# Kernel tuning notes

Measured on AMD Instinct MI355X. Metric: run time of the kernel, lower is better.

Reference implementation:

```python
import jax, jax.numpy as jnp
import numpy as np

N = 2048      # n_nodes
D = 512       # n_channels
AVG_DEG = 16  # average graph degree


def setup_inputs() -> dict:
    key = jax.random.key(0)
    k1, k2, k3 = jax.random.split(key, 3)
    # node features [N, D]
    x = jax.random.normal(k1, (N, D), dtype=jnp.float32)
    # random symmetric graph -> combinatorial Laplacian L = D - A
    E = N * AVG_DEG
    src = jax.random.randint(k2, (E,), 0, N)
    dst = jax.random.randint(k3, (E,), 0, N)
    A = jnp.zeros((N, N), jnp.float32).at[src, dst].add(1.0)
    A = (A + A.T) * 0.5
    A = A * (1.0 - jnp.eye(N, dtype=jnp.float32))  # drop self loops
    deg = A.sum(axis=1)
    L = jnp.diag(deg) - A
    # learned diffusion time (scalar parameter, ic=0.5)
    t = jnp.float32(0.5)
    return {"x": x, "L": L, "t": t}


def reference(x, L, t):
    # forward clamps diffusion_time to >= 1e-8
    tt = jnp.maximum(t, jnp.float32(1e-8))
    # heat kernel: expm(-t * L); the original loops over channels applying
    # compute_diffusion(x[:, [i]], t, L, 'matrix_exp') == expm(-t L) @ x[:, i],
    # which is exactly one dense matmul fused across all channels.
    P = jax.scipy.linalg.expm(-tt * L)  # [N, N]
    return P @ x  # [N, D]
```

## Files before the change

### kernel.cpp

```cpp
#include <hip/hip_runtime.h>

#define N_NODES 2048
#define N_CH    512
#define K_CHEB  48
#define NB      256

#define OFF_DIAG   0
#define OFF_BASE   20480
#define OFF_CNTO   28672
#define OFF_BND    36868
#define OFF_PKV    40960

#define PAD_OFF    16384u

__device__ __forceinline__ float b2f(unsigned short u) {
    return __uint_as_float(((unsigned int)u) << 16);
}
__device__ __forceinline__ bool detect32(const unsigned int* tw) {
    return (tw[0] & 0xFFFFu) == 0u;
}

__global__ void __launch_bounds__(256)
k_prep(const void* __restrict__ Lp, const unsigned int* __restrict__ tw,
       float* __restrict__ diagv, int* __restrict__ basev, int* __restrict__ cnto,
       unsigned short* __restrict__ pkv, unsigned int* __restrict__ bnd) {
    __shared__ unsigned short stage[4][N_NODES];
    __shared__ int scnt[4];
    int w    = threadIdx.x >> 6;
    int lane = threadIdx.x & 63;
    int row  = blockIdx.x * 4 + w;
    if (blockIdx.x == 0 && threadIdx.x == 0) *bnd = 0u;
    bool is32 = detect32(tw);
    int run = 0; float dv = 0.f;
    if (is32) {
        const float4* rf4 = (const float4*)((const float*)Lp + (size_t)row * N_NODES);
        #pragma unroll
        for (int i = 0; i < 8; i++) {
            int j = i * 64 + lane;
            float4 v = rf4[j];
            if (j == (row >> 2)) {
                int rm = row & 3;
                if      (rm == 0) { dv = v.x; v.x = 0.f; }
                else if (rm == 1) { dv = v.y; v.y = 0.f; }
                else if (rm == 2) { dv = v.z; v.z = 0.f; }
                else              { dv = v.w; v.w = 0.f; }
            }
            int c0 = j * 4;
            int n0 = (v.x != 0.f) ? (int)(-2.0f * v.x + 0.5f) : 0;
            int n1 = (v.y != 0.f) ? (int)(-2.0f * v.y + 0.5f) : 0;
            int n2 = (v.z != 0.f) ? (int)(-2.0f * v.z + 0.5f) : 0;
            int n3 = (v.w != 0.f) ? (int)(-2.0f * v.w + 0.5f) : 0;
            int tn = n0 + n1 + n2 + n3;
            int xs = tn;
            #pragma unroll
            for (int d = 1; d < 64; d <<= 1) { int q = __shfl_up(xs, d); if (lane >= d) xs += q; }
            int o = run + xs - tn;
            for (int q = 0; q < n0; q++) stage[w][o++] = (unsigned short)((c0 + 0) << 3);
            for (int q = 0; q < n1; q++) stage[w][o++] = (unsigned short)((c0 + 1) << 3);
            for (int q = 0; q < n2; q++) stage[w][o++] = (unsigned short)((c0 + 2) << 3);
            for (int q = 0; q < n3; q++) stage[w][o++] = (unsigned short)((c0 + 3) << 3);
            run += __shfl(xs, 63);
        }
    } else {
        const unsigned short* rp = (const unsigned short*)Lp + (size_t)row * N_NODES;
        for (int c0 = 0; c0 < N_NODES; c0 += 64) {
            float v = b2f(rp[c0 + lane]);
            int n = 0;
            if (c0 + lane == row) dv = v;
            else if (v != 0.f)    n = (int)(-2.0f * v + 0.5f);
            int xs = n;
            #pragma unroll
            for (int d = 1; d < 64; d <<= 1) { int q = __shfl_up(xs, d); if (lane >= d) xs += q; }
            int o = run + xs - n;
            for (int q = 0; q < n; q++) stage[w][o + q] = (unsigned short)((c0 + lane) << 3);
            run += __shfl(xs, 63);
        }
    }
    #pragma unroll
    for (int o = 32; o; o >>= 1) dv += __shfl_xor(dv, o);
    int padded = (run + 7) & ~7;
    for (int e = run + lane; e < padded; e += 64) stage[w][e] = (unsigned short)PAD_OFF;
    if (lane == 0) scnt[w] = padded;
    __syncthreads();
    int myb = blockIdx.x * 256;
    for (int w2 = 0; w2 < w; w2++) myb += scnt[w2];
    if (lane == 0) { basev[row] = myb; cnto[row] = padded >> 3; diagv[row] = dv; }
    const unsigned int* s32 = (const unsigned int*)stage[w];
    unsigned int* p32 = (unsigned int*)pkv + (myb >> 1);
    for (int i = lane; i < (padded >> 1); i += 64) p32[i] = s32[i];
}

__global__ void __launch_bounds__(256)
k_bound(const float* __restrict__ diagv, const int* __restrict__ basev,
        const int* __restrict__ cnto, const unsigned short* __restrict__ pkv,
        unsigned int* __restrict__ bnd) {
    __shared__ float wmax[4];
    int w    = threadIdx.x >> 6;
    int lane = threadIdx.x & 63;
    int r    = blockIdx.x * 4 + w;
    float d = diagv[r];
    float mb = 0.f;
    if (d > 0.f) {
        const unsigned short* pe = pkv + basev[r];
        int cnt = cnto[r] << 3;
        float s = 0.f;
        for (int e = lane; e < cnt; e += 64) {
            unsigned int u = pe[e];
            if (u < PAD_OFF) s += diagv[u >> 3];
        }
        #pragma unroll
        for (int o = 32; o; o >>= 1) s += __shfl_xor(s, o);
        mb = d + 0.5f * s / d;
    }
    if (lane == 0) wmax[w] = mb;
    __syncthreads();
    if (threadIdx.x == 0) {
        float m = fmaxf(fmaxf(wmax[0], wmax[1]), fmaxf(wmax[2], wmax[3]));
        atomicMax(bnd, __float_as_uint(m));
    }
}

__device__ __forceinline__ void oct_acc(const float2* __restrict__ cur, uint4 q,
                                        float& ax, float& ay, float& bx, float& by) {
    const char* cb = (const char*)cur;
    #pragma unroll
    for (int i = 0; i < 4; i++) {
        unsigned int u = (i == 0) ? q.x : (i == 1) ? q.y : (i == 2) ? q.z : q.w;
        float2 c0 = *(const float2*)(cb + (u & 0xFFFFu));
        float2 c1 = *(const float2*)(cb + (u >> 16));
        ax += c0.x; ay += c0.y;
        bx += c1.x; by += c1.y;
    }
}

__device__ __forceinline__ float2 gatherR(const float2* __restrict__ cur,
                                          const uint4* __restrict__ s4,
                                          int j0, int j1) {
    float ax = 0.f, ay = 0.f, bx = 0.f, by = 0.f;
    int j = j0;
    if (j + 2 <= j1) {
        uint4 q0 = s4[j], q1 = s4[j + 1];
        j += 2;
        while (j + 2 <= j1) {
            uint4 p0 = s4[j], p1 = s4[j + 1];
            oct_acc(cur, q0, ax, ay, bx, by);
            oct_acc(cur, q1, ax, ay, bx, by);
            q0 = p0; q1 = p1;
            j += 2;
        }
        oct_acc(cur, q0, ax, ay, bx, by);
        oct_acc(cur, q1, ax, ay, bx, by);
    }
    if (j < j1) oct_acc(cur, s4[j], ax, ay, bx, by);
    return make_float2(ax + bx, ay + by);
}

__global__ void __launch_bounds__(1024, 4)
k_cheb(const void* __restrict__ x, const unsigned int* __restrict__ tw,
       const int* __restrict__ basev, const int* __restrict__ cnto,
       const float* __restrict__ diagv, const unsigned short* __restrict__ pkv,
       const unsigned int* __restrict__ bnd, void* __restrict__ out) {
    __shared__ float2 bufA[N_NODES + 8];
    __shared__ float2 bufB[N_NODES + 8];
    __shared__ float  scoef[K_CHEB + 1];
    __shared__ float  cabs[K_CHEB + 1];
    __shared__ int    permL[N_NODES];
    __shared__ int    waveCnt[16][32];
    __shared__ int    wavePre[16][32];
    __shared__ int    hstart[32];
    __shared__ float  sred[16];
    __shared__ double dzs;
    __shared__ float  gss;
    __shared__ int    kks;

    int t    = threadIdx.x;
    int lane = t & 63;
    int wid  = t >> 6;
    int cb   = blockIdx.x * 2;
    bool is32 = detect32(tw);
    if (t == 0) {
        bufA[N_NODES] = make_float2(0.f, 0.f);
        bufB[N_NODES] = make_float2(0.f, 0.f);
    }
    int r0 = t, r1 = t + 1024;
    float mx = fmaxf(diagv[r0], diagv[r1]);
    int q0 = min(cnto[r0], 31), q1 = min(cnto[r1], 31);
    unsigned long long below = (1ull << lane) - 1ull;
    int rk0 = 0, rk1 = 0;
    #pragma unroll 1
    for (int k = 0; k < 32; k++) {
        unsigned long long m0 = __ballot(q0 == k);
        unsigned long long m1 = __ballot(q1 == k);
        if (q0 == k) rk0 = (int)__popcll(m0 & below);
        if (q1 == k) rk1 = (int)__popcll(m0) + (int)__popcll(m1 & below);
        if (lane == 0) waveCnt[wid][k] = (int)(__popcll(m0) + __popcll(m1));
    }
    #pragma unroll
    for (int o = 32; o; o >>= 1) mx = fmaxf(mx, __shfl_xor(mx, o));
    if (lane == 0) sred[wid] = mx;
    __syncthreads();
    if (t < 32) {
        int acc = 0;
        for (int w2 = 0; w2 < 16; w2++) { wavePre[w2][t] = acc; acc += waveCnt[w2][t]; }
        hstart[t] = acc;
    }
    __syncthreads();
    if (t == 0) {
        int acc = 0;
        for (int l = 31; l >= 0; l--) { int c = hstart[l]; hstart[l] = acc; acc += c; }
        float m = sred[0];
        #pragma unroll
        for (int i = 1; i < 16; i++) m = fmaxf(m, sred[i]);
        float tt = is32 ? __uint_as_float(tw[0]) : b2f((unsigned short)(tw[0] & 0xFFFFu));
        tt = fmaxf(tt, 1e-8f);
        float beta = 2.0f * m;
        float bM   = __uint_as_float(bnd[0]) * 1.00002f + 1e-7f;
        if (bM > 0.f && bM < beta) beta = bM;
        gss = (beta > 0.f) ? 2.0f / beta : 0.f;
        dzs = (beta > 0.f) ? (double)tt * (double)beta * 0.5 : 0.0;
    }
    __syncthreads();
    if (t <= K_CHEB) {
        int k = t;
        double z = dzs;
        double emz = exp(-z), h = 0.5 * z, h2 = h * h;
        double term = 1.0;
        for (int j = 1; j <= k; j++) term *= h / (double)j;
        double sum = term;
        for (int m = 1; m < 300; m++) {
            term *= h2 / ((double)m * (double)(m + k));
            sum += term;
            if (term == 0.0 || term < sum * 1e-18) break;
        }
        double ck = emz * sum * (k == 0 ? 1.0 : 2.0);
        if (k & 1) ck = -ck;
        scoef[k] = (float)ck;
        cabs[k]  = (float)fabs(ck);
    }
    permL[hstart[q0] + wavePre[wid][q0] + rk0] = r0;
    permL[hstart[q1] + wavePre[wid][q1] + rk1] = r1;
    __syncthreads();
    if (t == 0) {
        int keff = 1;
        for (int k = K_CHEB; k >= 2; k--)
            if (cabs[k] >= 2.5e-4f) { keff = k; break; }
        kks = keff;
    }
    __syncthreads();

    int ra = permL[t], rb = permL[2047 - t];
    int na = cnto[ra], nb = cnto[rb];
    int ja = basev[ra] >> 3, jb = basev[rb] >> 3;
    const uint4* s4 = (const uint4*)pkv;
    float da = diagv[ra], db = diagv[rb];
    float g = gss;
    int   K = kks;

    float2 xa, xb;
    if (is32) {
        xa = *(const float2*)((const float*)x + (size_t)ra * N_CH + cb);
        xb = *(const float2*)((const float*)x + (size_t)rb * N_CH + cb);
    } else {
        const unsigned short* xp = (const unsigned short*)x;
        unsigned int wa = *(const unsigned int*)(xp + (size_t)ra * N_CH + cb);
        unsigned int wb = *(const unsigned int*)(xp + (size_t)rb * N_CH + cb);
        xa = make_float2(b2f((unsigned short)(wa & 0xFFFFu)), b2f((unsigned short)(wa >> 16)));
        xb = make_float2(b2f((unsigned short)(wb & 0xFFFFu)), b2f((unsigned short)(wb >> 16)));
    }
    bufA[ra] = xa; bufA[rb] = xb;
    __syncthreads();

    float gm = -0.5f * g;
    float ia = g * da - 1.f, ib = g * db - 1.f;
    float2 aa = gatherR(bufA, s4, ja, ja + na);
    float2 ab = gatherR(bufA, s4, jb, jb + nb);
    float2 pva = xa, pvb = xb;
    float2 cua = make_float2(gm * aa.x + ia * xa.x, gm * aa.y + ia * xa.y);
    float2 cub = make_float2(gm * ab.x + ib * xb.x, gm * ab.y + ib * xb.y);
    float c0 = scoef[0], c1 = scoef[1];
    float2 oa = make_float2(c0 * xa.x + c1 * cua.x, c0 * xa.y + c1 * cua.y);
    float2 ob = make_float2(c0 * xb.x + c1 * cub.x, c0 * xb.y + c1 * cub.y);
    bufB[ra] = cua; bufB[rb] = cub;
    __syncthreads();

    float gn  = -g;
    float dga = 2.f * g * da - 2.f, dgb = 2.f * g * db - 2.f;

#define CHEB_STEP(RD, WR)                                                  \
    {   float ck = scoef[k];                                               \
        float2 ba = gatherR(RD, s4, ja, ja + na);                          \
        float2 bb = gatherR(RD, s4, jb, jb + nb);                          \
        float2 tna = make_float2(gn * ba.x + dga * cua.x - pva.x,          \
                                 gn * ba.y + dga * cua.y - pva.y);         \
        float2 tnb = make_float2(gn * bb.x + dgb * cub.x - pvb.x,          \
                                 gn * bb.y + dgb * cub.y - pvb.y);         \
        pva = cua; cua = tna;                                              \
        pvb = cub; cub = tnb;                                              \
        oa.x += ck * tna.x; oa.y += ck * tna.y;                            \
        ob.x += ck * tnb.x; ob.y += ck * tnb.y;                            \
        WR[ra] = tna; WR[rb] = tnb;                                        \
        __syncthreads(); }

    int k = 2;
    while (k <= K) {
        CHEB_STEP(bufB, bufA)
        k++;
        if (k > K) break;
        CHEB_STEP(bufA, bufB)
        k++;
    }
#undef CHEB_STEP

    if (is32) {
        *(float2*)((float*)out + (size_t)ra * N_CH + cb) = oa;
        *(float2*)((float*)out + (size_t)rb * N_CH + cb) = ob;
    } else {
        unsigned int ua, ub;
        { unsigned int u0 = __float_as_uint(oa.x), u1 = __float_as_uint(oa.y);
          u0 = (u0 + 0x7FFFu + ((u0 >> 16) & 1u)) >> 16;
          u1 = (u1 + 0x7FFFu + ((u1 >> 16) & 1u)) >> 16;
          ua = u0 | (u1 << 16); }
        { unsigned int u0 = __float_as_uint(ob.x), u1 = __float_as_uint(ob.y);
          u0 = (u0 + 0x7FFFu + ((u0 >> 16) & 1u)) >> 16;
          u1 = (u1 + 0x7FFFu + ((u1 >> 16) & 1u)) >> 16;
          ub = u0 | (u1 << 16); }
        *(unsigned int*)((unsigned short*)out + (size_t)ra * N_CH + cb) = ua;
        *(unsigned int*)((unsigned short*)out + (size_t)rb * N_CH + cb) = ub;
    }
}

extern "C" void kernel_launch(void* const* d_in, const int* in_sizes, int n_in,
                              void* d_out, int out_size, void* d_ws, size_t ws_size,
                              hipStream_t stream) {
    const void* x  = d_in[0];
    const void* L  = d_in[1];
    const void* tp = d_in[2];
    const unsigned int* tw = (const unsigned int*)tp;

    char* ws = (char*)d_ws;
    float*          diagv = (float*)          (ws + OFF_DIAG);
    int*            basev = (int*)            (ws + OFF_BASE);
    int*            cnto  = (int*)            (ws + OFF_CNTO);
    unsigned int*   bnd   = (unsigned int*)   (ws + OFF_BND);
    unsigned short* pkv   = (unsigned short*) (ws + OFF_PKV);

    k_prep <<<512, 256, 0, stream>>>(L, tw, diagv, basev, cnto, pkv, bnd);
    k_bound<<<512, 256, 0, stream>>>(diagv, basev, cnto, pkv, bnd);
    k_cheb <<<NB, 1024, 0, stream>>>(x, tw, basev, cnto, diagv, pkv, bnd, d_out);
}
```

Before: 164.0 us.

## Fold spectral bound computation into Chebyshev kernel and remap channel blocks

Removes the separate k_bound launch and recomputes the Gershgorin-style spectral bound redundantly inside every k_cheb block, reduced with wave shuffles and shared memory instead of a global atomicMax. A zero sentinel is written at diagv[N_NODES] so pad entries index a zero diagonal. The channel-block mapping is also permuted so neighbouring blocks touch strided channel pairs. This saves one kernel launch and its dependency, at the cost of every block rereading the packed adjacency and diagonal before the main iteration.

```diff
diff --git a/kernel.cpp b/kernel.cpp
--- a/kernel.cpp
+++ b/kernel.cpp
@@ -8,7 +8,6 @@
 #define OFF_DIAG   0
 #define OFF_BASE   20480
 #define OFF_CNTO   28672
-#define OFF_BND    36868
 #define OFF_PKV    40960
 
 #define PAD_OFF    16384u
@@ -23,13 +22,13 @@
 __global__ void __launch_bounds__(256)
 k_prep(const void* __restrict__ Lp, const unsigned int* __restrict__ tw,
        float* __restrict__ diagv, int* __restrict__ basev, int* __restrict__ cnto,
-       unsigned short* __restrict__ pkv, unsigned int* __restrict__ bnd) {
+       unsigned short* __restrict__ pkv) {
     __shared__ unsigned short stage[4][N_NODES];
     __shared__ int scnt[4];
     int w    = threadIdx.x >> 6;
     int lane = threadIdx.x & 63;
     int row  = blockIdx.x * 4 + w;
-    if (blockIdx.x == 0 && threadIdx.x == 0) *bnd = 0u;
+    if (blockIdx.x == 0 && threadIdx.x == 0) diagv[N_NODES] = 0.f;
     bool is32 = detect32(tw);
     int run = 0; float dv = 0.f;
     if (is32) {
@@ -90,36 +89,6 @@
     for (int i = lane; i < (padded >> 1); i += 64) p32[i] = s32[i];
 }
 
-__global__ void __launch_bounds__(256)
-k_bound(const float* __restrict__ diagv, const int* __restrict__ basev,
-        const int* __restrict__ cnto, const unsigned short* __restrict__ pkv,
-        unsigned int* __restrict__ bnd) {
-    __shared__ float wmax[4];
-    int w    = threadIdx.x >> 6;
-    int lane = threadIdx.x & 63;
-    int r    = blockIdx.x * 4 + w;
-    float d = diagv[r];
-    float mb = 0.f;
-    if (d > 0.f) {
-        const unsigned short* pe = pkv + basev[r];
-        int cnt = cnto[r] << 3;
-        float s = 0.f;
-        for (int e = lane; e < cnt; e += 64) {
-            unsigned int u = pe[e];
-            if (u < PAD_OFF) s += diagv[u >> 3];
-        }
-        #pragma unroll
-        for (int o = 32; o; o >>= 1) s += __shfl_xor(s, o);
-        mb = d + 0.5f * s / d;
-    }
-    if (lane == 0) wmax[w] = mb;
-    __syncthreads();
-    if (threadIdx.x == 0) {
-        float m = fmaxf(fmaxf(wmax[0], wmax[1]), fmaxf(wmax[2], wmax[3]));
-        atomicMax(bnd, __float_as_uint(m));
-    }
-}
-
 __device__ __forceinline__ void oct_acc(const float2* __restrict__ cur, uint4 q,
                                         float& ax, float& ay, float& bx, float& by) {
     const char* cb = (const char*)cur;
@@ -159,7 +128,7 @@
 k_cheb(const void* __restrict__ x, const unsigned int* __restrict__ tw,
        const int* __restrict__ basev, const int* __restrict__ cnto,
        const float* __restrict__ diagv, const unsigned short* __restrict__ pkv,
-       const unsigned int* __restrict__ bnd, void* __restrict__ out) {
+       void* __restrict__ out) {
     __shared__ float2 bufA[N_NODES + 8];
     __shared__ float2 bufB[N_NODES + 8];
     __shared__ float  scoef[K_CHEB + 1];
@@ -169,6 +138,7 @@
     __shared__ int    wavePre[16][32];
     __shared__ int    hstart[32];
     __shared__ float  sred[16];
+    __shared__ float  sredM[16];
     __shared__ double dzs;
     __shared__ float  gss;
     __shared__ int    kks;
@@ -176,14 +146,15 @@
     int t    = threadIdx.x;
     int lane = t & 63;
     int wid  = t >> 6;
-    int cb   = blockIdx.x * 2;
+    int cb   = ((blockIdx.x & 31) << 4) | ((blockIdx.x >> 5) << 1);
     bool is32 = detect32(tw);
     if (t == 0) {
         bufA[N_NODES] = make_float2(0.f, 0.f);
         bufB[N_NODES] = make_float2(0.f, 0.f);
     }
     int r0 = t, r1 = t + 1024;
-    float mx = fmaxf(diagv[r0], diagv[r1]);
+    float d0v = diagv[r0], d1v = diagv[r1];
+    float mx = fmaxf(d0v, d1v);
     int q0 = min(cnto[r0], 31), q1 = min(cnto[r1], 31);
     unsigned long long below = (1ull << lane) - 1ull;
     int rk0 = 0, rk1 = 0;
@@ -195,9 +166,35 @@
         if (q1 == k) rk1 = (int)__popcll(m0) + (int)__popcll(m1 & below);
         if (lane == 0) waveCnt[wid][k] = (int)(__popcll(m0) + __popcll(m1));
     }
+    float mb = 0.f;
+    {
+        const uint4* pk4 = (const uint4*)pkv;
+        float s0 = 0.f, s1 = 0.f;
+        int j0 = basev[r0] >> 3, n0 = cnto[r0];
+        for (int j = 0; j < n0; j++) {
+            uint4 q = pk4[j0 + j];
+            s0 += diagv[(q.x & 0xFFFFu) >> 3] + diagv[q.x >> 19]
+                + diagv[(q.y & 0xFFFFu) >> 3] + diagv[q.y >> 19]
+                + diagv[(q.z & 0xFFFFu) >> 3] + diagv[q.z >> 19]
+                + diagv[(q.w & 0xFFFFu) >> 3] + diagv[q.w >> 19];
+        }
+        int j1 = basev[r1] >> 3, n1 = cnto[r1];
+        for (int j = 0; j < n1; j++) {
+            uint4 q = pk4[j1 + j];
+            s1 += diagv[(q.x & 0xFFFFu) >> 3] + diagv[q.x >> 19]
+                + diagv[(q.y & 0xFFFFu) >> 3] + diagv[q.y >> 19]
+                + diagv[(q.z & 0xFFFFu) >> 3] + diagv[q.z >> 19]
+                + diagv[(q.w & 0xFFFFu) >> 3] + diagv[q.w >> 19];
+        }
+        if (d0v > 0.f) mb = d0v + 0.5f * s0 / d0v;
+        if (d1v > 0.f) mb = fmaxf(mb, d1v + 0.5f * s1 / d1v);
+    }
     #pragma unroll
-    for (int o = 32; o; o >>= 1) mx = fmaxf(mx, __shfl_xor(mx, o));
-    if (lane == 0) sred[wid] = mx;
+    for (int o = 32; o; o >>= 1) {
+        mx = fmaxf(mx, __shfl_xor(mx, o));
+        mb = fmaxf(mb, __shfl_xor(mb, o));
+    }
+    if (lane == 0) { sred[wid] = mx; sredM[wid] = mb; }
     __syncthreads();
     if (t < 32) {
         int acc = 0;
@@ -208,13 +205,13 @@
     if (t == 0) {
         int acc = 0;
         for (int l = 31; l >= 0; l--) { int c = hstart[l]; hstart[l] = acc; acc += c; }
-        float m = sred[0];
+        float m = sred[0], mM = sredM[0];
         #pragma unroll
-        for (int i = 1; i < 16; i++) m = fmaxf(m, sred[i]);
+        for (int i = 1; i < 16; i++) { m = fmaxf(m, sred[i]); mM = fmaxf(mM, sredM[i]); }
         float tt = is32 ? __uint_as_float(tw[0]) : b2f((unsigned short)(tw[0] & 0xFFFFu));
         tt = fmaxf(tt, 1e-8f);
         float beta = 2.0f * m;
-        float bM   = __uint_as_float(bnd[0]) * 1.00002f + 1e-7f;
+        float bM   = mM * 1.00002f + 1e-7f;
         if (bM > 0.f && bM < beta) beta = bM;
         gss = (beta > 0.f) ? 2.0f / beta : 0.f;
         dzs = (beta > 0.f) ? (double)tt * (double)beta * 0.5 : 0.0;
@@ -341,10 +338,8 @@
     float*          diagv = (float*)          (ws + OFF_DIAG);
     int*            basev = (int*)            (ws + OFF_BASE);
     int*            cnto  = (int*)            (ws + OFF_CNTO);
-    unsigned int*   bnd   = (unsigned int*)   (ws + OFF_BND);
     unsigned short* pkv   = (unsigned short*) (ws + OFF_PKV);
 
-    k_prep <<<512, 256, 0, stream>>>(L, tw, diagv, basev, cnto, pkv, bnd);
-    k_bound<<<512, 256, 0, stream>>>(diagv, basev, cnto, pkv, bnd);
-    k_cheb <<<NB, 1024, 0, stream>>>(x, tw, basev, cnto, diagv, pkv, bnd, d_out);
-}
+    k_prep <<<512, 256, 0, stream>>>(L, tw, diagv, basev, cnto, pkv);
+    k_cheb <<<NB, 1024, 0, stream>>>(x, tw, basev, cnto, diagv, pkv, d_out);
+}
```

Result: no change. 166.4 us (+1.5%).
